# Performance work log

Measured on AMD Instinct MI355X. Metric: run time of the kernel, lower is better.

## Reference

```python
import jax, jax.numpy as jnp
import numpy as np

D_MODEL = 2048
NUM_HEADS = 16
HEAD_DIM = D_MODEL // NUM_HEADS
D_FF = 8192
EPS = 1e-6


def rmsnorm(x, w):
    return x * jax.lax.rsqrt(jnp.mean(x * x, axis=-1, keepdims=True) + EPS) * w


def setup_inputs() -> dict:
    key = jax.random.key(0)
    ks = jax.random.split(key, 8)
    B, S, D = 2, 2048, D_MODEL
    s = lambda d: 1.0 / np.sqrt(d)
    return {
        "x": jax.random.normal(ks[0], (B, S, D), dtype=jnp.float32),
        "w_qkv": jax.random.normal(ks[1], (D, 3 * D), dtype=jnp.float32) * s(D),
        "w_out": jax.random.normal(ks[2], (D, D), dtype=jnp.float32) * s(D),
        "w1": jax.random.normal(ks[3], (D, D_FF), dtype=jnp.float32) * s(D),
        "w2": jax.random.normal(ks[4], (D_FF, D), dtype=jnp.float32) * s(D_FF),
        "w3": jax.random.normal(ks[5], (D, D_FF), dtype=jnp.float32) * s(D),
        "g1": jnp.ones((D,), dtype=jnp.float32),
        "g2": jnp.ones((D,), dtype=jnp.float32),
    }


def attention(x, w_qkv, w_out):
    B, S, D = x.shape
    H, Hd = NUM_HEADS, HEAD_DIM
    qkv = (x @ w_qkv).reshape(B, S, 3, H, Hd)
    q = qkv[:, :, 0].transpose(0, 2, 1, 3)  # [B,H,S,Hd]
    k = qkv[:, :, 1].transpose(0, 2, 1, 3)
    v = qkv[:, :, 2].transpose(0, 2, 1, 3)
    scale = Hd ** -0.5
    attn = jnp.einsum("bhqd,bhkd->bhqk", q, k) * scale
    causal = jnp.tril(jnp.ones((S, S), dtype=bool))
    attn = jnp.where(causal, attn, -jnp.inf)
    attn = jax.nn.softmax(attn, axis=-1)
    out = jnp.einsum("bhqk,bhkd->bhqd", attn, v)
    out = out.transpose(0, 2, 1, 3).reshape(B, S, D)
    return out @ w_out


def ffn(x, w1, w2, w3):
    return (jax.nn.silu(x @ w1) * (x @ w3)) @ w2


def reference(x, w_qkv, w_out, w1, w2, w3, g1, g2):
    x = x + attention(rmsnorm(x, g1), w_qkv, w_out)
    return x + ffn(rmsnorm(x, g2), w1, w2, w3)
```

## Files before the change

### kernel.cpp

```cpp
#include <hip/hip_runtime.h>
#include <cstdint>
#include <cstddef>

typedef __bf16 bf16x8 __attribute__((ext_vector_type(8)));
typedef float f32x4 __attribute__((ext_vector_type(4)));

__device__ __forceinline__ void gl_lds16(const void* g, void* l) {
  __builtin_amdgcn_global_load_lds(
      (const __attribute__((address_space(1))) void*)g,
      (__attribute__((address_space(3))) void*)l, 16, 0, 0);
}

__global__ __launch_bounds__(256) void wconv_t_k(const float* __restrict__ W,
                                                 __bf16* __restrict__ WT,
                                                 int K, int N) {
  __shared__ float tile[32][33];
  const int c0 = blockIdx.x * 32, r0 = blockIdx.y * 32;
  const int tx = threadIdx.x & 31, ty = threadIdx.x >> 5;
#pragma unroll
  for (int i = 0; i < 32; i += 8)
    tile[ty + i][tx] = W[(size_t)(r0 + ty + i) * N + c0 + tx];
  __syncthreads();
#pragma unroll
  for (int i = 0; i < 32; i += 8)
    WT[(size_t)(c0 + ty + i) * K + r0 + tx] = (__bf16)tile[tx][ty + i];
}

__global__ __launch_bounds__(256) void rmsnorm_k(const float* __restrict__ x,
                                                 const float* __restrict__ g,
                                                 __bf16* __restrict__ out) {
  constexpr int D = 2048;
  const int row = blockIdx.x, t = threadIdx.x;
  const float4* xr = (const float4*)(x + (size_t)row * D);
  float4 a = xr[t * 2], b2 = xr[t * 2 + 1];
  float ss = a.x * a.x + a.y * a.y + a.z * a.z + a.w * a.w +
             b2.x * b2.x + b2.y * b2.y + b2.z * b2.z + b2.w * b2.w;
#pragma unroll
  for (int d = 1; d < 64; d <<= 1) ss += __shfl_xor(ss, d, 64);
  __shared__ float red[4];
  if ((t & 63) == 0) red[t >> 6] = ss;
  __syncthreads();
  float rs = rsqrtf((red[0] + red[1] + red[2] + red[3]) * (1.f / D) + 1e-6f);
  const float4* gr = (const float4*)g;
  float4 ga = gr[t * 2], gb = gr[t * 2 + 1];
  bf16x8 o8;
  o8[0] = (__bf16)(a.x * rs * ga.x);
  o8[1] = (__bf16)(a.y * rs * ga.y);
  o8[2] = (__bf16)(a.z * rs * ga.z);
  o8[3] = (__bf16)(a.w * rs * ga.w);
  o8[4] = (__bf16)(b2.x * rs * gb.x);
  o8[5] = (__bf16)(b2.y * rs * gb.y);
  o8[6] = (__bf16)(b2.z * rs * gb.z);
  o8[7] = (__bf16)(b2.w * rs * gb.w);
  *(bf16x8*)(out + (size_t)row * D + t * 8) = o8;
}

__global__ __launch_bounds__(256) void addred_k(const float* __restrict__ p0,
                                                const float* __restrict__ p1,
                                                const float* __restrict__ res,
                                                float* __restrict__ out, int n4) {
  int i = blockIdx.x * 256 + threadIdx.x;
  const int stride = gridDim.x * 256;
  for (; i < n4; i += stride) {
    float4 a = ((const float4*)p0)[i];
    float4 b = ((const float4*)p1)[i];
    float4 c = ((const float4*)res)[i];
    float4 o = {a.x + b.x + c.x, a.y + b.y + c.y, a.z + b.z + c.z, a.w + b.w + c.w};
    ((float4*)out)[i] = o;
  }
}

#define RD_A(BUF, HALF) do {                                        \
  const __bf16* aT_ = &As[BUF][0] + aoff + (HALF) * 4096;           \
  _Pragma("unroll")                                                 \
  for (int mi = 0; mi < 4; ++mi) {                                  \
    Ar[mi][0] = *(const bf16x8*)(aT_ + mi * 1024 + k0off);          \
    Ar[mi][1] = *(const bf16x8*)(aT_ + mi * 1024 + k1off);          \
  } } while (0)

#define RD_B(BUF, NH) do {                                          \
  const __bf16* bT_ = &Bs[BUF][0] + boff + (NH) * 2048;             \
  _Pragma("unroll")                                                 \
  for (int ni = 0; ni < 2; ++ni) {                                  \
    Br[NH][ni][0] = *(const bf16x8*)(bT_ + ni * 1024 + k0off);      \
    Br[NH][ni][1] = *(const bf16x8*)(bT_ + ni * 1024 + k1off);      \
  } } while (0)

#define MQ(MH, NH) do {                                             \
  _Pragma("unroll")                                                 \
  for (int mi = 0; mi < 4; ++mi) {                                  \
    _Pragma("unroll")                                               \
    for (int ni = 0; ni < 2; ++ni) {                                \
      f32x4& a_ = acc[(MH) * 4 + mi][(NH) * 2 + ni];                \
      a_ = __builtin_amdgcn_mfma_f32_16x16x32_bf16(Ar[mi][0], Br[NH][ni][0], a_, 0, 0, 0); \
      a_ = __builtin_amdgcn_mfma_f32_16x16x32_bf16(Ar[mi][1], Br[NH][ni][1], a_, 0, 0, 0); \
    } } } while (0)

#define PH_MID() do {                                               \
  __builtin_amdgcn_sched_barrier(0);                                \
  __builtin_amdgcn_s_barrier();                                     \
  asm volatile("s_waitcnt lgkmcnt(0)" ::: "memory");                \
  __builtin_amdgcn_sched_barrier(0);                                \
  __builtin_amdgcn_s_setprio(1);                                    \
} while (0)

#define PH_END(VM) do {                                             \
  __builtin_amdgcn_s_setprio(0);                                    \
  asm volatile("s_waitcnt vmcnt(" #VM ")" ::: "memory");            \
  __builtin_amdgcn_sched_barrier(0);                                \
  __builtin_amdgcn_s_barrier();                                     \
} while (0)

#define PH_END_NOVM() do {                                          \
  __builtin_amdgcn_s_setprio(0);                                    \
  __builtin_amdgcn_s_barrier();                                     \
} while (0)

#define KTILE(BUF, STG0, STG1, STG2, STG3, END0, END1, END3) do {   \
  RD_A(BUF, 0); RD_B(BUF, 0); STG0; PH_MID(); MQ(0, 0); END0;       \
  RD_B(BUF, 1);               STG1; PH_MID(); MQ(0, 1); END1;       \
  RD_A(BUF, 1);               STG2; PH_MID(); MQ(1, 1); PH_END_NOVM(); \
                              STG3; PH_MID(); MQ(1, 0); END3;       \
} while (0)

template <int MODE>
__global__ __launch_bounds__(512, 2) void gemm8_k(
    const __bf16* __restrict__ A, const __bf16* __restrict__ BT,
    const float* __restrict__ res, const __bf16* __restrict__ aux,
    void* __restrict__ Cout, int M, int N, int K, int lda, int cswz) {
  __shared__ alignas(16) __bf16 As[2][256 * 64];
  __shared__ alignas(16) __bf16 Bs[2][256 * 64];
  const int tid = threadIdx.x;
  const int lane = tid & 63, w = tid >> 6;
  const int wm = w >> 2, wn = w & 3;
  const int l15 = lane & 15, l16 = lane >> 4;

  const int nbx = gridDim.x, nby = gridDim.y;
  const int nwg = nbx * nby;
  const int bid = blockIdx.y * nbx + blockIdx.x;
  const int swz = (bid & 7) * (nwg >> 3) + (bid >> 3);
  int bx, by;
  if (cswz) { by = swz % nby; bx = swz / nby; }
  else      { bx = swz % nbx; by = swz / nbx; }
  const int m0 = by * 256, n0 = bx * 256;
  const int nkt = K >> 6;

  float* CoutF = (float*)Cout;
  if constexpr (MODE == 4) {
    const int z = blockIdx.z;
    A += (size_t)z * K;
    BT += (size_t)z * K;
    CoutF += (size_t)z * M * N;
  }

  const int srow = tid >> 3;
  const int scole = ((tid & 7) * 8) ^ ((srow & 7) << 3);
  const int brow_i = ((tid >> 8) << 6) + ((tid >> 3) & 31);

  auto stgA = [&](int t, int h) {
    if (t < nkt) {
      char* dst = (char*)(&As[t & 1][0]) + h * 8192 + tid * 16;
      const __bf16* src = A + (size_t)(m0 + h * 64 + srow) * lda + t * 64 + scole;
      gl_lds16(src, dst);
      gl_lds16(src + (size_t)128 * lda, dst + 16384);
    }
  };
  auto stgB = [&](int t, int h) {
    if (t < nkt) {
      const int r = h * 32 + brow_i;
      char* dst = (char*)(&Bs[t & 1][0]) + r * 128 + (tid & 7) * 16;
      const __bf16* src = BT + (size_t)(n0 + r) * lda + t * 64 + scole;
      gl_lds16(src, dst);
      gl_lds16(src + (size_t)128 * lda, dst + 16384);
    }
  };

  const int rswz = (l15 & 7) << 3;
  const int k0off = (l16 * 8) ^ rswz;
  const int k1off = (32 + l16 * 8) ^ rswz;
  const int aoff = (wm * 128 + l15) * 64;
  const int boff = (wn * 64 + l15) * 64;

  f32x4 acc[8][4] = {};
  bf16x8 Ar[4][2], Br[2][2][2];

  stgA(0, 0); stgB(0, 0); stgB(0, 1); stgA(0, 1);
  stgA(1, 0); stgB(1, 0);
  asm volatile("s_waitcnt vmcnt(8)" ::: "memory");
  __builtin_amdgcn_s_barrier();

  int t = 0;
  for (; t + 3 < nkt; t += 2) {
    KTILE(0, stgB(t + 1, 1), stgA(t + 1, 1), stgA(t + 2, 0), stgB(t + 2, 0),
          PH_END(8), PH_END(8), PH_END(8));
    KTILE(1, stgB(t + 2, 1), stgA(t + 2, 1), stgA(t + 3, 0), stgB(t + 3, 0),
          PH_END(8), PH_END(8), PH_END(8));
  }
  KTILE(0, stgB(t + 1, 1), stgA(t + 1, 1), (void)0, (void)0,
        PH_END(8), PH_END(8), PH_END(4));
  KTILE(1, (void)0, (void)0, (void)0, (void)0,
        PH_END(2), PH_END(0), __builtin_amdgcn_s_setprio(0));

#pragma unroll
  for (int m = 0; m < 8; ++m) {
    const int rowb = m0 + wm * 128 + m * 16 + l16 * 4;
#pragma unroll
    for (int n = 0; n < 4; ++n) {
      const int col = n0 + wn * 64 + n * 16 + l15;
#pragma unroll
      for (int r = 0; r < 4; ++r) {
        const size_t idx = (size_t)(rowb + r) * N + col;
        float v = acc[m][n][r];
        if constexpr (MODE == 1) {
          CoutF[idx] = v + res[idx];
        } else if constexpr (MODE == 2) {
          float s = v / (1.f + __expf(-v));
          ((__bf16*)Cout)[idx] = (__bf16)s;
        } else if constexpr (MODE == 3) {
          ((__bf16*)Cout)[idx] = (__bf16)(v * (float)aux[idx]);
        } else if constexpr (MODE == 4) {
          CoutF[idx] = v;
        } else {
          ((__bf16*)Cout)[idx] = (__bf16)v;
        }
      }
    }
  }
}

__global__ __launch_bounds__(256) void vtrans_k(const __bf16* __restrict__ qkv,
                                                __bf16* __restrict__ VT) {
  constexpr int S = 2048;
  __shared__ __bf16 tile[64][65];
  const int s0 = blockIdx.x * 64, d0 = blockIdx.y * 64;
  const int bh = blockIdx.z, b = bh >> 4, h = bh & 15;
  const int tx = threadIdx.x & 63, ty = threadIdx.x >> 6;
  const size_t vbase = ((size_t)b * S * 3 + 2) * 2048 + h * 128;
#pragma unroll
  for (int i = 0; i < 16; ++i) {
    int s = ty + i * 4;
    tile[s][tx] = qkv[vbase + (size_t)(s0 + s) * 6144 + d0 + tx];
  }
  __syncthreads();
  const size_t obase = ((size_t)bh * 128 + d0) * S + s0;
#pragma unroll
  for (int i = 0; i < 16; ++i) {
    int d = ty + i * 4;
    VT[obase + (size_t)d * S + tx] = tile[tx][d];
  }
}

__global__ __launch_bounds__(256) void attn_k(const __bf16* __restrict__ qkv,
                                              const __bf16* __restrict__ VT,
                                              __bf16* __restrict__ out) {
  constexpr int S = 2048;
  const int bid = blockIdx.x;
  const int bh = (bid & 7) * 4 + ((bid >> 3) & 3);
  const int qb = 31 - (bid >> 5);
  const int b = bh >> 4, h = bh & 15;
  const int q0 = qb * 64;
  const int tid = threadIdx.x, lane = tid & 63, w = tid >> 6;
  const int l15 = lane & 15, l16 = lane >> 4;

  __shared__ __bf16 Ks[64 * 128];
  __shared__ __bf16 Vs[128 * 64];
  __shared__ __bf16 Ps[4][16 * 72];

  const size_t qbase = (size_t)b * S * 6144 + h * 128;
  const size_t kbase = qbase + 2048;
  const size_t vtbase = (size_t)bh * 128 * 2048;

  bf16x8 qf[4];
  {
    const __bf16* qp = qkv + qbase + (size_t)(q0 + w * 16 + l15) * 6144 + l16 * 8;
#pragma unroll
    for (int kc = 0; kc < 4; ++kc) qf[kc] = *(const bf16x8*)(qp + kc * 32);
  }

  f32x4 o[8] = {};
  float mrow[4] = {-1e30f, -1e30f, -1e30f, -1e30f};
  float lrow[4] = {0.f, 0.f, 0.f, 0.f};
  const float sm = 0.08838834764831845f * 1.4426950408889634f;

  int ksrow[4], kscol[4], vsrow[4], vscol[4];
#pragma unroll
  for (int c = 0; c < 4; ++c) {
    int P = (c * 256 + tid) * 16;
    int kr = P >> 8;
    ksrow[c] = kr;
    kscol[c] = ((P & 255) ^ ((kr & 7) << 4)) >> 1;
    int vr = P >> 7;
    vsrow[c] = vr;
    vscol[c] = ((P & 127) ^ ((vr & 7) << 4)) >> 1;
  }
  const int fswz = (l15 & 7) << 3;
  const int qrow_abs = q0 + w * 16 + l16 * 4;

#pragma unroll
  for (int c = 0; c < 4; ++c) {
    int e = (c * 256 + tid) * 8;
    gl_lds16(qkv + kbase + (size_t)ksrow[c] * 6144 + kscol[c], &Ks[e]);
    gl_lds16(VT + vtbase + (size_t)vsrow[c] * 2048 + vscol[c], &Vs[e]);
  }

  for (int kt = 0; kt <= qb; ++kt) {
    const int k0 = kt * 64;
    __syncthreads();

    bf16x8 kreg[4], vreg[4];
    const bool pf = kt < qb;
    if (pf) {
      const int kn = k0 + 64;
#pragma unroll
      for (int c = 0; c < 4; ++c)
        kreg[c] = *(const bf16x8*)(qkv + kbase + (size_t)(kn + ksrow[c]) * 6144 + kscol[c]);
#pragma unroll
      for (int c = 0; c < 4; ++c)
        vreg[c] = *(const bf16x8*)(VT + vtbase + (size_t)vsrow[c] * 2048 + kn + vscol[c]);
    }

    f32x4 s4[4];
    __builtin_amdgcn_s_setprio(1);
#pragma unroll
    for (int f = 0; f < 4; ++f) {
      f32x4 accs = {};
#pragma unroll
      for (int kc = 0; kc < 4; ++kc) {
        bf16x8 kf = *(const bf16x8*)&Ks[(f * 16 + l15) * 128 + ((kc * 32 + l16 * 8) ^ fswz)];
        accs = __builtin_amdgcn_mfma_f32_16x16x32_bf16(qf[kc], kf, accs, 0, 0, 0);
      }
      s4[f] = accs;
    }
    __builtin_amdgcn_s_setprio(0);

    float pm[4] = {-1e30f, -1e30f, -1e30f, -1e30f};
    float pvv[4][4];
#pragma unroll
    for (int f = 0; f < 4; ++f) {
      const int key = k0 + f * 16 + l15;
#pragma unroll
      for (int r = 0; r < 4; ++r) {
        float s = s4[f][r] * sm;
        if (key > qrow_abs + r) s = -1e30f;
        pvv[f][r] = s;
        pm[r] = fmaxf(pm[r], s);
      }
    }
#pragma unroll
    for (int d = 1; d < 16; d <<= 1) {
#pragma unroll
      for (int r = 0; r < 4; ++r) pm[r] = fmaxf(pm[r], __shfl_xor(pm[r], d, 64));
    }
    float fac[4], ts[4];
#pragma unroll
    for (int r = 0; r < 4; ++r) {
      float mn = fmaxf(mrow[r], pm[r]);
      fac[r] = exp2f(mrow[r] - mn);
      mrow[r] = mn;
      ts[r] = 0.f;
    }
#pragma unroll
    for (int f = 0; f < 4; ++f) {
#pragma unroll
      for (int r = 0; r < 4; ++r) {
        float p = exp2f(pvv[f][r] - mrow[r]);
        ts[r] += p;
        Ps[w][(l16 * 4 + r) * 72 + f * 16 + l15] = (__bf16)p;
      }
    }
#pragma unroll
    for (int d = 1; d < 16; d <<= 1) {
#pragma unroll
      for (int r = 0; r < 4; ++r) ts[r] += __shfl_xor(ts[r], d, 64);
    }
#pragma unroll
    for (int r = 0; r < 4; ++r) lrow[r] = lrow[r] * fac[r] + ts[r];
#pragma unroll
    for (int n = 0; n < 8; ++n) {
      o[n][0] *= fac[0];
      o[n][1] *= fac[1];
      o[n][2] *= fac[2];
      o[n][3] *= fac[3];
    }
    __builtin_amdgcn_s_setprio(1);
#pragma unroll
    for (int kc = 0; kc < 2; ++kc) {
      bf16x8 pf2 = *(const bf16x8*)&Ps[w][l15 * 72 + kc * 32 + l16 * 8];
#pragma unroll
      for (int n = 0; n < 8; ++n) {
        bf16x8 vf = *(const bf16x8*)&Vs[(n * 16 + l15) * 64 + ((kc * 32 + l16 * 8) ^ fswz)];
        o[n] = __builtin_amdgcn_mfma_f32_16x16x32_bf16(pf2, vf, o[n], 0, 0, 0);
      }
    }
    __builtin_amdgcn_s_setprio(0);
    __syncthreads();

    if (pf) {
#pragma unroll
      for (int c = 0; c < 4; ++c) *(bf16x8*)&Ks[(c * 256 + tid) * 8] = kreg[c];
#pragma unroll
      for (int c = 0; c < 4; ++c) *(bf16x8*)&Vs[(c * 256 + tid) * 8] = vreg[c];
    }
  }

  const int orow = b * S + q0 + w * 16 + l16 * 4;
#pragma unroll
  for (int r = 0; r < 4; ++r) {
    const float inv = 1.f / lrow[r];
#pragma unroll
    for (int n = 0; n < 8; ++n)
      out[(size_t)(orow + r) * 2048 + h * 128 + n * 16 + l15] = (__bf16)(o[n][r] * inv);
  }
}

extern "C" void kernel_launch(void* const* d_in, const int* in_sizes, int n_in,
                              void* d_out, int out_size, void* d_ws, size_t ws_size,
                              hipStream_t stream) {
  (void)in_sizes; (void)n_in; (void)out_size; (void)ws_size;
  const float* x = (const float*)d_in[0];
  const float* w_qkv = (const float*)d_in[1];
  const float* w_out = (const float*)d_in[2];
  const float* w1 = (const float*)d_in[3];
  const float* w2 = (const float*)d_in[4];
  const float* w3 = (const float*)d_in[5];
  const float* g1 = (const float*)d_in[6];
  const float* g2 = (const float*)d_in[7];
  char* ws = (char*)d_ws;

  constexpr int Mr = 4096, D = 2048, DFF = 8192, TD = 6144;

  __bf16* wqkvT = (__bf16*)(ws + 0);
  __bf16* w1T   = (__bf16*)(ws + 0);
  __bf16* woutT = (__bf16*)(ws + 33554432);
  __bf16* qkvb  = (__bf16*)(ws + 41943040);
  __bf16* w3T   = (__bf16*)(ws + 41943040);
  __bf16* w2T   = (__bf16*)(ws + 75497472);
  __bf16* VTb   = (__bf16*)(ws + 92274688);
  __bf16* xn    = (__bf16*)(ws + 109051904);
  __bf16* attn  = (__bf16*)(ws + 125829120);
  float*  hbuf  = (float*)(ws + 142606336);
  __bf16* gbuf  = (__bf16*)(ws + 176160768);
  float*  pO    = (float*)(ws + 176160768);
  float*  pW0   = (float*)(ws + 0);

  wconv_t_k<<<dim3(TD / 32, D / 32), 256, 0, stream>>>(w_qkv, wqkvT, D, TD);
  wconv_t_k<<<dim3(D / 32, D / 32), 256, 0, stream>>>(w_out, woutT, D, D);
  rmsnorm_k<<<Mr, 256, 0, stream>>>(x, g1, xn);
  gemm8_k<0><<<dim3(TD / 256, Mr / 256), 512, 0, stream>>>(xn, wqkvT, nullptr, nullptr, qkvb, Mr, TD, D, D, 1);
  vtrans_k<<<dim3(32, 2, 32), 256, 0, stream>>>(qkvb, VTb);
  attn_k<<<1024, 256, 0, stream>>>(qkvb, VTb, attn);
  gemm8_k<4><<<dim3(D / 256, Mr / 256, 2), 512, 0, stream>>>(attn, woutT, nullptr, nullptr, pO, Mr, D, D / 2, D, 0);
  addred_k<<<2048, 256, 0, stream>>>(pO, pO + (size_t)Mr * D, x, hbuf, Mr * D / 4);
  rmsnorm_k<<<Mr, 256, 0, stream>>>(hbuf, g2, xn);
  wconv_t_k<<<dim3(DFF / 32, D / 32), 256, 0, stream>>>(w1, w1T, D, DFF);
  wconv_t_k<<<dim3(DFF / 32, D / 32), 256, 0, stream>>>(w3, w3T, D, DFF);
  wconv_t_k<<<dim3(D / 32, DFF / 32), 256, 0, stream>>>(w2, w2T, DFF, D);
  gemm8_k<2><<<dim3(DFF / 256, Mr / 256), 512, 0, stream>>>(xn, w1T, nullptr, nullptr, gbuf, Mr, DFF, D, D, 1);
  gemm8_k<3><<<dim3(DFF / 256, Mr / 256), 512, 0, stream>>>(xn, w3T, nullptr, gbuf, gbuf, Mr, DFF, D, D, 1);
  gemm8_k<4><<<dim3(D / 256, Mr / 256, 2), 512, 0, stream>>>(gbuf, w2T, nullptr, nullptr, pW0, Mr, D, DFF / 2, DFF, 0);
  addred_k<<<2048, 256, 0, stream>>>(pW0, pW0 + (size_t)Mr * D, hbuf, (float*)d_out, Mr * D / 4);
}
```

Before: 761.6 us.

## Fuse W1/W3 FFN GEMMs into one kernel and merge residual add with RMSNorm

```diff
diff --git a/kernel.cpp b/kernel.cpp
--- a/kernel.cpp
+++ b/kernel.cpp
@@ -3,6 +3,7 @@
 #include <cstddef>
 
 typedef __bf16 bf16x8 __attribute__((ext_vector_type(8)));
+typedef __bf16 bf16x4 __attribute__((ext_vector_type(4)));
 typedef float f32x4 __attribute__((ext_vector_type(4)));
 
 __device__ __forceinline__ void gl_lds16(const void* g, void* l) {
@@ -55,6 +56,47 @@
   *(bf16x8*)(out + (size_t)row * D + t * 8) = o8;
 }
 
+__global__ __launch_bounds__(256) void addrms_k(const float* __restrict__ p0,
+                                                const float* __restrict__ p1,
+                                                const float* __restrict__ res,
+                                                const float* __restrict__ g,
+                                                float* __restrict__ hout,
+                                                __bf16* __restrict__ xnout) {
+  constexpr int D = 2048;
+  const int row = blockIdx.x, t = threadIdx.x;
+  const size_t base = (size_t)row * D;
+  float4 h[2];
+#pragma unroll
+  for (int j = 0; j < 2; ++j) {
+    float4 a = ((const float4*)(p0 + base))[t * 2 + j];
+    float4 b = ((const float4*)(p1 + base))[t * 2 + j];
+    float4 c = ((const float4*)(res + base))[t * 2 + j];
+    h[j].x = a.x + b.x + c.x; h[j].y = a.y + b.y + c.y;
+    h[j].z = a.z + b.z + c.z; h[j].w = a.w + b.w + c.w;
+    ((float4*)(hout + base))[t * 2 + j] = h[j];
+  }
+  float ss = h[0].x * h[0].x + h[0].y * h[0].y + h[0].z * h[0].z + h[0].w * h[0].w +
+             h[1].x * h[1].x + h[1].y * h[1].y + h[1].z * h[1].z + h[1].w * h[1].w;
+#pragma unroll
+  for (int d = 1; d < 64; d <<= 1) ss += __shfl_xor(ss, d, 64);
+  __shared__ float red[4];
+  if ((t & 63) == 0) red[t >> 6] = ss;
+  __syncthreads();
+  float rs = rsqrtf((red[0] + red[1] + red[2] + red[3]) * (1.f / D) + 1e-6f);
+  const float4* gr = (const float4*)g;
+  float4 ga = gr[t * 2], gb = gr[t * 2 + 1];
+  bf16x8 o8;
+  o8[0] = (__bf16)(h[0].x * rs * ga.x);
+  o8[1] = (__bf16)(h[0].y * rs * ga.y);
+  o8[2] = (__bf16)(h[0].z * rs * ga.z);
+  o8[3] = (__bf16)(h[0].w * rs * ga.w);
+  o8[4] = (__bf16)(h[1].x * rs * gb.x);
+  o8[5] = (__bf16)(h[1].y * rs * gb.y);
+  o8[6] = (__bf16)(h[1].z * rs * gb.z);
+  o8[7] = (__bf16)(h[1].w * rs * gb.w);
+  *(bf16x8*)(xnout + base + t * 8) = o8;
+}
+
 __global__ __launch_bounds__(256) void addred_k(const float* __restrict__ p0,
                                                 const float* __restrict__ p1,
                                                 const float* __restrict__ res,
@@ -123,18 +165,61 @@
                               STG3; PH_MID(); MQ(1, 0); END3;       \
 } while (0)
 
+#define GEMM_SETUP(APTR, LDA_)                                            \
+  const int tid = threadIdx.x;                                            \
+  const int lane = tid & 63, w = tid >> 6;                                \
+  const int wm = w >> 2, wn = w & 3;                                      \
+  const int l15 = lane & 15, l16 = lane >> 4;                             \
+  const int lda = (LDA_);                                                 \
+  const int srow = tid >> 3;                                              \
+  const int scole = ((tid & 7) * 8) ^ ((srow & 7) << 3);                  \
+  const int brow_i = ((tid >> 8) << 6) + ((tid >> 3) & 31);               \
+  const int laneAoff = (m0 + srow) * lda + scole;                         \
+  const int laneBoff = (n0 + brow_i) * lda + scole;                       \
+  const int adst = tid * 16;                                              \
+  const int bdst = brow_i * 128 + (tid & 7) * 16;                         \
+  const int rswz = (l15 & 7) << 3;                                        \
+  const int k0off = (l16 * 8) ^ rswz;                                     \
+  const int k1off = (32 + l16 * 8) ^ rswz;                                \
+  const int aoff = (wm * 128 + l15) * 64;                                 \
+  const int boff = (wn * 64 + l15) * 64;                                  \
+  auto stgA = [&](int t, int h) {                                         \
+    char* dst = (char*)(&As[t & 1][0]) + h * 8192 + adst;                 \
+    const __bf16* srcU = (APTR) + (size_t)t * 64 + (size_t)(h * 64) * lda;\
+    gl_lds16(srcU + laneAoff, dst);                                       \
+    gl_lds16(srcU + laneAoff + (size_t)128 * lda, dst + 16384);           \
+  };                                                                      \
+  auto stgB = [&](int t, int h) {                                         \
+    char* dst = (char*)(&Bs[t & 1][0]) + h * 4096 + bdst;                 \
+    const __bf16* srcU = btp + (size_t)t * 64 + (size_t)(h * 32) * lda;   \
+    gl_lds16(srcU + laneBoff, dst);                                       \
+    gl_lds16(srcU + laneBoff + (size_t)128 * lda, dst + 16384);           \
+  };
+
+#define GEMM_PIPELINE() do {                                              \
+  stgA(0, 0); stgB(0, 0); stgB(0, 1); stgA(0, 1);                         \
+  stgA(1, 0); stgB(1, 0);                                                 \
+  asm volatile("s_waitcnt vmcnt(8)" ::: "memory");                        \
+  __builtin_amdgcn_s_barrier();                                           \
+  int t = 0;                                                              \
+  for (; t + 3 < nkt; t += 2) {                                           \
+    KTILE(0, stgB(t + 1, 1), stgA(t + 1, 1), stgA(t + 2, 0), stgB(t + 2, 0), \
+          PH_END(8), PH_END(8), PH_END(8));                               \
+    KTILE(1, stgB(t + 2, 1), stgA(t + 2, 1), stgA(t + 3, 0), stgB(t + 3, 0), \
+          PH_END(8), PH_END(8), PH_END(8));                               \
+  }                                                                       \
+  KTILE(0, stgB(t + 1, 1), stgA(t + 1, 1), (void)0, (void)0,              \
+        PH_END(8), PH_END(8), PH_END(4));                                 \
+  KTILE(1, (void)0, (void)0, (void)0, (void)0,                            \
+        PH_END(2), PH_END(0), __builtin_amdgcn_s_setprio(0));             \
+} while (0)
+
 template <int MODE>
 __global__ __launch_bounds__(512, 2) void gemm8_k(
     const __bf16* __restrict__ A, const __bf16* __restrict__ BT,
-    const float* __restrict__ res, const __bf16* __restrict__ aux,
-    void* __restrict__ Cout, int M, int N, int K, int lda, int cswz) {
+    void* __restrict__ Cout, int M, int N, int K, int lda_p, int cswz) {
   __shared__ alignas(16) __bf16 As[2][256 * 64];
   __shared__ alignas(16) __bf16 Bs[2][256 * 64];
-  const int tid = threadIdx.x;
-  const int lane = tid & 63, w = tid >> 6;
-  const int wm = w >> 2, wn = w & 3;
-  const int l15 = lane & 15, l16 = lane >> 4;
-
   const int nbx = gridDim.x, nby = gridDim.y;
   const int nwg = nbx * nby;
   const int bid = blockIdx.y * nbx + blockIdx.x;
@@ -152,54 +237,12 @@
     BT += (size_t)z * K;
     CoutF += (size_t)z * M * N;
   }
-
-  const int srow = tid >> 3;
-  const int scole = ((tid & 7) * 8) ^ ((srow & 7) << 3);
-  const int brow_i = ((tid >> 8) << 6) + ((tid >> 3) & 31);
-
-  auto stgA = [&](int t, int h) {
-    if (t < nkt) {
-      char* dst = (char*)(&As[t & 1][0]) + h * 8192 + tid * 16;
-      const __bf16* src = A + (size_t)(m0 + h * 64 + srow) * lda + t * 64 + scole;
-      gl_lds16(src, dst);
-      gl_lds16(src + (size_t)128 * lda, dst + 16384);
-    }
-  };
-  auto stgB = [&](int t, int h) {
-    if (t < nkt) {
-      const int r = h * 32 + brow_i;
-      char* dst = (char*)(&Bs[t & 1][0]) + r * 128 + (tid & 7) * 16;
-      const __bf16* src = BT + (size_t)(n0 + r) * lda + t * 64 + scole;
-      gl_lds16(src, dst);
-      gl_lds16(src + (size_t)128 * lda, dst + 16384);
-    }
-  };
-
-  const int rswz = (l15 & 7) << 3;
-  const int k0off = (l16 * 8) ^ rswz;
-  const int k1off = (32 + l16 * 8) ^ rswz;
-  const int aoff = (wm * 128 + l15) * 64;
-  const int boff = (wn * 64 + l15) * 64;
+  const __bf16* btp = BT;
+  GEMM_SETUP(A, lda_p);
 
   f32x4 acc[8][4] = {};
   bf16x8 Ar[4][2], Br[2][2][2];
-
-  stgA(0, 0); stgB(0, 0); stgB(0, 1); stgA(0, 1);
-  stgA(1, 0); stgB(1, 0);
-  asm volatile("s_waitcnt vmcnt(8)" ::: "memory");
-  __builtin_amdgcn_s_barrier();
-
-  int t = 0;
-  for (; t + 3 < nkt; t += 2) {
-    KTILE(0, stgB(t + 1, 1), stgA(t + 1, 1), stgA(t + 2, 0), stgB(t + 2, 0),
-          PH_END(8), PH_END(8), PH_END(8));
-    KTILE(1, stgB(t + 2, 1), stgA(t + 2, 1), stgA(t + 3, 0), stgB(t + 3, 0),
-          PH_END(8), PH_END(8), PH_END(8));
-  }
-  KTILE(0, stgB(t + 1, 1), stgA(t + 1, 1), (void)0, (void)0,
-        PH_END(8), PH_END(8), PH_END(4));
-  KTILE(1, (void)0, (void)0, (void)0, (void)0,
-        PH_END(2), PH_END(0), __builtin_amdgcn_s_setprio(0));
+  GEMM_PIPELINE();
 
 #pragma unroll
   for (int m = 0; m < 8; ++m) {
@@ -210,19 +253,62 @@
 #pragma unroll
       for (int r = 0; r < 4; ++r) {
         const size_t idx = (size_t)(rowb + r) * N + col;
-        float v = acc[m][n][r];
-        if constexpr (MODE == 1) {
-          CoutF[idx] = v + res[idx];
-        } else if constexpr (MODE == 2) {
-          float s = v / (1.f + __expf(-v));
-          ((__bf16*)Cout)[idx] = (__bf16)s;
-        } else if constexpr (MODE == 3) {
-          ((__bf16*)Cout)[idx] = (__bf16)(v * (float)aux[idx]);
-        } else if constexpr (MODE == 4) {
-          CoutF[idx] = v;
-        } else {
-          ((__bf16*)Cout)[idx] = (__bf16)v;
-        }
+        if constexpr (MODE == 4) CoutF[idx] = acc[m][n][r];
+        else ((__bf16*)Cout)[idx] = (__bf16)acc[m][n][r];
+      }
+    }
+  }
+}
+
+__global__ __launch_bounds__(512, 2) void ffn8_k(
+    const __bf16* __restrict__ A, const __bf16* __restrict__ B1T,
+    const __bf16* __restrict__ B3T, __bf16* __restrict__ Cout,
+    int M, int N, int K, int lda_p) {
+  __shared__ alignas(16) __bf16 As[2][256 * 64];
+  __shared__ alignas(16) __bf16 Bs[2][256 * 64];
+  const int nbx = gridDim.x, nby = gridDim.y;
+  const int nwg = nbx * nby;
+  const int bid = blockIdx.y * nbx + blockIdx.x;
+  const int swz = (bid & 7) * (nwg >> 3) + (bid >> 3);
+  const int by = swz % nby, bx = swz / nby;
+  const int m0 = by * 256, n0 = bx * 256;
+  const int nkt = K >> 6;
+
+  const __bf16* btp = B3T;
+  GEMM_SETUP(A, lda_p);
+
+  f32x4 acc[8][4] = {};
+  bf16x8 Ar[4][2], Br[2][2][2];
+
+  GEMM_PIPELINE();
+
+  bf16x4 gs[8][4];
+#pragma unroll
+  for (int m = 0; m < 8; ++m)
+#pragma unroll
+    for (int n = 0; n < 4; ++n) {
+      bf16x4 v;
+      v[0] = (__bf16)acc[m][n][0]; v[1] = (__bf16)acc[m][n][1];
+      v[2] = (__bf16)acc[m][n][2]; v[3] = (__bf16)acc[m][n][3];
+      gs[m][n] = v;
+      acc[m][n] = (f32x4){0.f, 0.f, 0.f, 0.f};
+    }
+  __syncthreads();
+
+  btp = B1T;
+  GEMM_PIPELINE();
+
+#pragma unroll
+  for (int m = 0; m < 8; ++m) {
+    const int rowb = m0 + wm * 128 + m * 16 + l16 * 4;
+#pragma unroll
+    for (int n = 0; n < 4; ++n) {
+      const int col = n0 + wn * 64 + n * 16 + l15;
+#pragma unroll
+      for (int r = 0; r < 4; ++r) {
+        float a = acc[m][n][r];
+        float s = a / (1.f + __expf(-a));
+        Cout[(size_t)(rowb + r) * N + col] = (__bf16)(s * (float)gs[m][n][r]);
       }
     }
   }
@@ -446,17 +532,15 @@
   wconv_t_k<<<dim3(TD / 32, D / 32), 256, 0, stream>>>(w_qkv, wqkvT, D, TD);
   wconv_t_k<<<dim3(D / 32, D / 32), 256, 0, stream>>>(w_out, woutT, D, D);
   rmsnorm_k<<<Mr, 256, 0, stream>>>(x, g1, xn);
-  gemm8_k<0><<<dim3(TD / 256, Mr / 256), 512, 0, stream>>>(xn, wqkvT, nullptr, nullptr, qkvb, Mr, TD, D, D, 1);
+  gemm8_k<0><<<dim3(TD / 256, Mr / 256), 512, 0, stream>>>(xn, wqkvT, qkvb, Mr, TD, D, D, 1);
   vtrans_k<<<dim3(32, 2, 32), 256, 0, stream>>>(qkvb, VTb);
   attn_k<<<1024, 256, 0, stream>>>(qkvb, VTb, attn);
-  gemm8_k<4><<<dim3(D / 256, Mr / 256, 2), 512, 0, stream>>>(attn, woutT, nullptr, nullptr, pO, Mr, D, D / 2, D, 0);
-  addred_k<<<2048, 256, 0, stream>>>(pO, pO + (size_t)Mr * D, x, hbuf, Mr * D / 4);
-  rmsnorm_k<<<Mr, 256, 0, stream>>>(hbuf, g2, xn);
+  gemm8_k<4><<<dim3(D / 256, Mr / 256, 2), 512, 0, stream>>>(attn, woutT, pO, Mr, D, D / 2, D, 0);
+  addrms_k<<<Mr, 256, 0, stream>>>(pO, pO + (size_t)Mr * D, x, g2, hbuf, xn);
   wconv_t_k<<<dim3(DFF / 32, D / 32), 256, 0, stream>>>(w1, w1T, D, DFF);
   wconv_t_k<<<dim3(DFF / 32, D / 32), 256, 0, stream>>>(w3, w3T, D, DFF);
   wconv_t_k<<<dim3(D / 32, DFF / 32), 256, 0, stream>>>(w2, w2T, DFF, D);
-  gemm8_k<2><<<dim3(DFF / 256, Mr / 256), 512, 0, stream>>>(xn, w1T, nullptr, nullptr, gbuf, Mr, DFF, D, D, 1);
-  gemm8_k<3><<<dim3(DFF / 256, Mr / 256), 512, 0, stream>>>(xn, w3T, nullptr, gbuf, gbuf, Mr, DFF, D, D, 1);
-  gemm8_k<4><<<dim3(D / 256, Mr / 256, 2), 512, 0, stream>>>(gbuf, w2T, nullptr, nullptr, pW0, Mr, D, DFF / 2, DFF, 0);
+  ffn8_k<<<dim3(DFF / 256, Mr / 256), 512, 0, stream>>>(xn, w1T, w3T, gbuf, Mr, DFF, D, D);
+  gemm8_k<4><<<dim3(D / 256, Mr / 256, 2), 512, 0, stream>>>(gbuf, w2T, pW0, Mr, D, DFF / 2, DFF, 0);
   addred_k<<<2048, 256, 0, stream>>>(pW0, pW0 + (size_t)Mr * D, hbuf, (float*)d_out, Mr * D / 4);
 }
```

After: 967.4 us. 27.0% more time.

## Enlarge attention query tile to 128 rows and fuse residual add with RMSNorm

Applied to the files above, without the earlier changes.

```diff
diff --git a/kernel.cpp b/kernel.cpp
--- a/kernel.cpp
+++ b/kernel.cpp
@@ -55,6 +55,47 @@
   *(bf16x8*)(out + (size_t)row * D + t * 8) = o8;
 }
 
+__global__ __launch_bounds__(256) void addrms_k(const float* __restrict__ p0,
+                                                const float* __restrict__ p1,
+                                                const float* __restrict__ res,
+                                                const float* __restrict__ g,
+                                                float* __restrict__ hout,
+                                                __bf16* __restrict__ xnout) {
+  constexpr int D = 2048;
+  const int row = blockIdx.x, t = threadIdx.x;
+  const size_t base = (size_t)row * D;
+  float4 h[2];
+#pragma unroll
+  for (int j = 0; j < 2; ++j) {
+    float4 a = ((const float4*)(p0 + base))[t * 2 + j];
+    float4 b = ((const float4*)(p1 + base))[t * 2 + j];
+    float4 c = ((const float4*)(res + base))[t * 2 + j];
+    h[j].x = a.x + b.x + c.x; h[j].y = a.y + b.y + c.y;
+    h[j].z = a.z + b.z + c.z; h[j].w = a.w + b.w + c.w;
+    ((float4*)(hout + base))[t * 2 + j] = h[j];
+  }
+  float ss = h[0].x * h[0].x + h[0].y * h[0].y + h[0].z * h[0].z + h[0].w * h[0].w +
+             h[1].x * h[1].x + h[1].y * h[1].y + h[1].z * h[1].z + h[1].w * h[1].w;
+#pragma unroll
+  for (int d = 1; d < 64; d <<= 1) ss += __shfl_xor(ss, d, 64);
+  __shared__ float red[4];
+  if ((t & 63) == 0) red[t >> 6] = ss;
+  __syncthreads();
+  float rs = rsqrtf((red[0] + red[1] + red[2] + red[3]) * (1.f / D) + 1e-6f);
+  const float4* gr = (const float4*)g;
+  float4 ga = gr[t * 2], gb = gr[t * 2 + 1];
+  bf16x8 o8;
+  o8[0] = (__bf16)(h[0].x * rs * ga.x);
+  o8[1] = (__bf16)(h[0].y * rs * ga.y);
+  o8[2] = (__bf16)(h[0].z * rs * ga.z);
+  o8[3] = (__bf16)(h[0].w * rs * ga.w);
+  o8[4] = (__bf16)(h[1].x * rs * gb.x);
+  o8[5] = (__bf16)(h[1].y * rs * gb.y);
+  o8[6] = (__bf16)(h[1].z * rs * gb.z);
+  o8[7] = (__bf16)(h[1].w * rs * gb.w);
+  *(bf16x8*)(xnout + base + t * 8) = o8;
+}
+
 __global__ __launch_bounds__(256) void addred_k(const float* __restrict__ p0,
                                                 const float* __restrict__ p1,
                                                 const float* __restrict__ res,
@@ -250,21 +291,21 @@
   }
 }
 
-__global__ __launch_bounds__(256) void attn_k(const __bf16* __restrict__ qkv,
+__global__ __launch_bounds__(512) void attn_k(const __bf16* __restrict__ qkv,
                                               const __bf16* __restrict__ VT,
                                               __bf16* __restrict__ out) {
   constexpr int S = 2048;
   const int bid = blockIdx.x;
   const int bh = (bid & 7) * 4 + ((bid >> 3) & 3);
-  const int qb = 31 - (bid >> 5);
+  const int qb = 15 - (bid >> 5);
   const int b = bh >> 4, h = bh & 15;
-  const int q0 = qb * 64;
+  const int q0 = qb * 128;
   const int tid = threadIdx.x, lane = tid & 63, w = tid >> 6;
   const int l15 = lane & 15, l16 = lane >> 4;
 
   __shared__ __bf16 Ks[64 * 128];
   __shared__ __bf16 Vs[128 * 64];
-  __shared__ __bf16 Ps[4][16 * 72];
+  __shared__ __bf16 Ps[8][16 * 72];
 
   const size_t qbase = (size_t)b * S * 6144 + h * 128;
   const size_t kbase = qbase + 2048;
@@ -282,10 +323,10 @@
   float lrow[4] = {0.f, 0.f, 0.f, 0.f};
   const float sm = 0.08838834764831845f * 1.4426950408889634f;
 
-  int ksrow[4], kscol[4], vsrow[4], vscol[4];
-#pragma unroll
-  for (int c = 0; c < 4; ++c) {
-    int P = (c * 256 + tid) * 16;
+  int ksrow[2], kscol[2], vsrow[2], vscol[2];
+#pragma unroll
+  for (int c = 0; c < 2; ++c) {
+    int P = (c * 512 + tid) * 16;
     int kr = P >> 8;
     ksrow[c] = kr;
     kscol[c] = ((P & 255) ^ ((kr & 7) << 4)) >> 1;
@@ -297,25 +338,26 @@
   const int qrow_abs = q0 + w * 16 + l16 * 4;
 
 #pragma unroll
-  for (int c = 0; c < 4; ++c) {
-    int e = (c * 256 + tid) * 8;
+  for (int c = 0; c < 2; ++c) {
+    int e = (c * 512 + tid) * 8;
     gl_lds16(qkv + kbase + (size_t)ksrow[c] * 6144 + kscol[c], &Ks[e]);
     gl_lds16(VT + vtbase + (size_t)vsrow[c] * 2048 + vscol[c], &Vs[e]);
   }
 
-  for (int kt = 0; kt <= qb; ++kt) {
+  const int ntk = 2 * qb + 2;
+  for (int kt = 0; kt < ntk; ++kt) {
     const int k0 = kt * 64;
     __syncthreads();
 
-    bf16x8 kreg[4], vreg[4];
-    const bool pf = kt < qb;
+    bf16x8 kreg[2], vreg[2];
+    const bool pf = kt + 1 < ntk;
     if (pf) {
       const int kn = k0 + 64;
 #pragma unroll
-      for (int c = 0; c < 4; ++c)
+      for (int c = 0; c < 2; ++c)
         kreg[c] = *(const bf16x8*)(qkv + kbase + (size_t)(kn + ksrow[c]) * 6144 + kscol[c]);
 #pragma unroll
-      for (int c = 0; c < 4; ++c)
+      for (int c = 0; c < 2; ++c)
         vreg[c] = *(const bf16x8*)(VT + vtbase + (size_t)vsrow[c] * 2048 + kn + vscol[c]);
     }
 
@@ -397,9 +439,9 @@
 
     if (pf) {
 #pragma unroll
-      for (int c = 0; c < 4; ++c) *(bf16x8*)&Ks[(c * 256 + tid) * 8] = kreg[c];
-#pragma unroll
-      for (int c = 0; c < 4; ++c) *(bf16x8*)&Vs[(c * 256 + tid) * 8] = vreg[c];
+      for (int c = 0; c < 2; ++c) *(bf16x8*)&Ks[(c * 512 + tid) * 8] = kreg[c];
+#pragma unroll
+      for (int c = 0; c < 2; ++c) *(bf16x8*)&Vs[(c * 512 + tid) * 8] = vreg[c];
     }
   }
 
@@ -448,10 +490,9 @@
   rmsnorm_k<<<Mr, 256, 0, stream>>>(x, g1, xn);
   gemm8_k<0><<<dim3(TD / 256, Mr / 256), 512, 0, stream>>>(xn, wqkvT, nullptr, nullptr, qkvb, Mr, TD, D, D, 1);
   vtrans_k<<<dim3(32, 2, 32), 256, 0, stream>>>(qkvb, VTb);
-  attn_k<<<1024, 256, 0, stream>>>(qkvb, VTb, attn);
+  attn_k<<<512, 512, 0, stream>>>(qkvb, VTb, attn);
   gemm8_k<4><<<dim3(D / 256, Mr / 256, 2), 512, 0, stream>>>(attn, woutT, nullptr, nullptr, pO, Mr, D, D / 2, D, 0);
-  addred_k<<<2048, 256, 0, stream>>>(pO, pO + (size_t)Mr * D, x, hbuf, Mr * D / 4);
-  rmsnorm_k<<<Mr, 256, 0, stream>>>(hbuf, g2, xn);
+  addrms_k<<<Mr, 256, 0, stream>>>(pO, pO + (size_t)Mr * D, x, g2, hbuf, xn);
   wconv_t_k<<<dim3(DFF / 32, D / 32), 256, 0, stream>>>(w1, w1T, D, DFF);
   wconv_t_k<<<dim3(DFF / 32, D / 32), 256, 0, stream>>>(w3, w3T, D, DFF);
   wconv_t_k<<<dim3(D / 32, DFF / 32), 256, 0, stream>>>(w2, w2T, DFF, D);
```

Result: no change. 752.7 us (-1.2%).
